# Performance work log

Hardware: AMD Instinct MI355X
Metric: run time of the kernel (lower is better)

## Reference

```python
import jax, jax.numpy as jnp
import numpy as np

ALPHA = 0.15
CLIP = 5.0
EPS = 1e-6
LN_EPS = 1e-5

B, S, D, F = 4, 4096, 2048, 128


def setup_inputs() -> dict:
    key = jax.random.key(0)
    ks = jax.random.split(key, 8)
    sd = lambda fan_in: 1.0 / np.sqrt(fan_in)
    return {
        "x": jax.random.normal(ks[0], (B, S, D), dtype=jnp.float32),
        "Q_w": jax.random.normal(ks[1], (D, F), dtype=jnp.float32) * sd(D),
        "Q_b": jnp.zeros((F,), jnp.float32),
        "K_w": jax.random.normal(ks[2], (D, F), dtype=jnp.float32) * sd(D),
        "K_b": jnp.zeros((F,), jnp.float32),
        "lo_proj_w": jax.random.normal(ks[3], (D, D), dtype=jnp.float32) * sd(D),
        "lo_proj_b": jnp.zeros((D,), jnp.float32),
        "lo_p_w": jax.random.normal(ks[4], (D, F), dtype=jnp.float32) * sd(D),
        "lo_p_b": jnp.zeros((F,), jnp.float32),
        "proj_w": jax.random.normal(ks[5], (F, D), dtype=jnp.float32) * sd(F),
        "proj_b": jnp.zeros((D,), jnp.float32),
        "O_w": jax.random.normal(ks[6], (D // 2, D), dtype=jnp.float32) * sd(D // 2),
        "O_b": jnp.zeros((D,), jnp.float32),
        "ln_gamma": jnp.ones((D,), jnp.float32),
        "ln_beta": jnp.zeros((D,), jnp.float32),
    }


def _ema_over_time(score):
    # score: [B, S, F]; ema[0]=score[0]; ema[t]=a*score[t]+(1-a)*ema[t-1]
    seq = jnp.swapaxes(score, 0, 1)  # [S, B, F]

    def step(prev, x_t):
        new = ALPHA * x_t + (1.0 - ALPHA) * prev
        return new, new

    init = seq[0]
    _, rest = jax.lax.scan(step, init, seq[1:])
    ema_seq = jnp.concatenate([init[None], rest], axis=0)
    return jnp.swapaxes(ema_seq, 0, 1)


def reference(x, Q_w, Q_b, K_w, K_b, lo_proj_w, lo_proj_b, lo_p_w, lo_p_b,
              proj_w, proj_b, O_w, O_b, ln_gamma, ln_beta):
    x_f32 = x.astype(jnp.float32)
    residual = x_f32

    q = x_f32 @ Q_w + Q_b                    # [B,S,128]
    k = x_f32 @ K_w + K_b                    # [B,S,128]
    # Lo: Dense(d_model) -> gelu -> Dense(128)
    v_h = jax.nn.gelu(x_f32 @ lo_proj_w + lo_proj_b)
    V = v_h @ lo_p_w + lo_p_b                # [B,S,128]

    score = jax.nn.sigmoid(q) * jax.nn.sigmoid(k)
    score_ema = _ema_over_time(score)
    mean_last = jnp.mean(score_ema, axis=-1, keepdims=True)
    denom = jnp.maximum(mean_last, EPS)
    score_clipped = jnp.clip(score_ema / denom, -CLIP, CLIP)

    x_comb = score_clipped * V               # [B,S,128]
    out = x_comb @ proj_w + proj_b           # [B,S,D]  (D even -> no pad)
    a, b = jnp.split(out, 2, axis=-1)
    gated = jax.nn.silu(a) * b               # [B,S,D/2]
    out = gated @ O_w + O_b                  # [B,S,D]

    h = out + residual
    mu = jnp.mean(h, axis=-1, keepdims=True)
    var = jnp.var(h, axis=-1, keepdims=True)
    out = (h - mu) * jax.lax.rsqrt(var + LN_EPS) * ln_gamma + ln_beta
    return out.astype(x.dtype)
```

## Files before the change

kernel.cpp:

```cpp
#include <hip/hip_runtime.h>
#include <cstdint>

#define ALPHA_C 0.15f
#define ONE_MINUS_ALPHA 0.85f
#define CLIP_C 5.0f
#define EPS_C 1e-6f
#define LN_EPS_C 1e-5f

#define Bb 4
#define Ss 4096
#define Dd 2048
#define Mtot (Bb * Ss)

typedef __attribute__((ext_vector_type(8))) short bf16x8;
typedef __attribute__((ext_vector_type(4))) float f32x4;

__device__ __forceinline__ short f2bf(float f) {
  union { float f; uint32_t u; } v; v.f = f;
  uint32_t r = v.u + 0x7fffu + ((v.u >> 16) & 1u);
  return (short)(r >> 16);
}
__device__ __forceinline__ float sigf(float x) { return 1.0f / (1.0f + __expf(-x)); }
__device__ __forceinline__ float geluf(float x) {
  const float c = 0.7978845608028654f;
  float x3 = x * x * x;
  return 0.5f * x * (1.0f + tanhf(c * (x + 0.044715f * x3)));
}

__device__ __forceinline__ void load_lds16(const short* g, short* l) {
  __builtin_amdgcn_global_load_lds((__attribute__((address_space(1))) void*)g,
                                   (__attribute__((address_space(3))) void*)l, 16, 0, 0);
}


#define RD_A(MH, KK)                                                                 \
  _Pragma("unroll") for (int mm = 0; mm < 4; ++mm)                                   \
      a[mm] = *(const bf16x8*)&Ab[(wr128 + ((MH) * 4 + mm) * 16 + l16) * 64 +        \
                                  ((((KK) * 4 + quad) ^ key) * 8)];
#define RD_B(KK)                                                                     \
  _Pragma("unroll") for (int nn = 0; nn < 4; ++nn)                                   \
      bq[nn] = *(const bf16x8*)&Bl[(wc64 + nn * 16 + l16) * 64 +                     \
                                   ((((KK) * 4 + quad) ^ key) * 8)];
#define MFMA_Q(MH)                                                                   \
  __builtin_amdgcn_s_setprio(1);                                                     \
  _Pragma("unroll") for (int mm = 0; mm < 4; ++mm)                                   \
  _Pragma("unroll") for (int nn = 0; nn < 4; ++nn)                                   \
      acc[(MH) * 4 + mm][nn] = __builtin_amdgcn_mfma_f32_16x16x32_bf16(              \
          a[mm], bq[nn], acc[(MH) * 4 + mm][nn], 0, 0, 0);                           \
  __builtin_amdgcn_s_setprio(0);
#define BARF()                                                                       \
  {                                                                                  \
    asm volatile("" ::: "memory");                                                   \
    __builtin_amdgcn_s_barrier();                                                    \
    asm volatile("" ::: "memory");                                                   \
  }
#define STAGE_HALF_A(TT, H)                                                          \
  {                                                                                  \
    short* ls = smem + ((TT) & 1) * 32768 + (H) * 8192;                              \
    const long co = (long)(TT) * 64;                                                 \
    load_lds16(baseA + ((H) * 128 + 0) * (long)lda + co, ls + w * 512);              \
    load_lds16(baseA + ((H) * 128 + 64) * (long)lda + co, ls + 4096 + w * 512);      \
  }
#define STAGE_HALF_B(TT, H)                                                          \
  {                                                                                  \
    short* ls = smem + ((TT) & 1) * 32768 + 16384 + (H) * 8192;                      \
    const long co = (long)(TT) * 64;                                                 \
    load_lds16(baseB + ((H) * 128 + 0) * (long)ldb + co, ls + w * 512);              \
    load_lds16(baseB + ((H) * 128 + 64) * (long)ldb + co, ls + 4096 + w * 512);      \
  }

#define TILE_BODY(CB, STG, TN)                                                       \
  {                                                                                  \
    const short* Ab = smem + (CB) * 32768;                                           \
    const short* Bl = Ab + 16384;                                                    \
                                                                  \
    if (STG) {                                                                       \
      STAGE_HALF_A(TN, 0);                                                           \
      asm volatile("s_waitcnt vmcnt(2)" ::: "memory");                               \
    } else {                                                                         \
      asm volatile("s_waitcnt vmcnt(0)" ::: "memory");                               \
    }                                                                                \
    __builtin_amdgcn_s_barrier();                                                    \
    asm volatile("" ::: "memory");                                                   \
    RD_A(0, 0);                                                                      \
    RD_B(0);                                                                         \
    asm volatile("s_waitcnt lgkmcnt(0)" ::: "memory");                               \
    MFMA_Q(0);                                                                       \
    BARF();                                                                          \
                                                                        \
    RD_A(1, 0);                                                                      \
    if (STG) STAGE_HALF_A(TN, 1);                                                    \
    __builtin_amdgcn_s_barrier();                                                    \
    asm volatile("s_waitcnt lgkmcnt(0)" ::: "memory");                               \
    MFMA_Q(1);                                                                       \
    BARF();                                                                          \
                                                                        \
    RD_A(0, 1);                                                                      \
    RD_B(1);                                                                         \
    if (STG) STAGE_HALF_B(TN, 0);                                                    \
    __builtin_amdgcn_s_barrier();                                                    \
    asm volatile("s_waitcnt lgkmcnt(0)" ::: "memory");                               \
    MFMA_Q(0);                                                                       \
    BARF();                                                                          \
                                                                        \
    RD_A(1, 1);                                                                      \
    if (STG) STAGE_HALF_B(TN, 1);                                                    \
    __builtin_amdgcn_s_barrier();                                                    \
    asm volatile("s_waitcnt lgkmcnt(0)" ::: "memory");                               \
    MFMA_Q(1);                                                                       \
    BARF();                                                                          \
  }

template <int MODE>
__global__ __launch_bounds__(512, 2) void gemm256(
    const short* __restrict__ A, const short* __restrict__ Bt, void* __restrict__ out0,
    void* __restrict__ out1, const float* __restrict__ bias, int K, int lda, int ldb,
    int ldc, int nbx) {
  __shared__ short smem[65536];

  const int tid = threadIdx.x;
  const int w = tid >> 6;
  const int lane = tid & 63;
  const int quad = lane >> 4;
  const int l16 = lane & 15;
  const int key = l16 & 7;
  const int wr = w >> 2;
  const int wc = w & 3;
  const int wr128 = wr * 128;
  const int wc64 = wc * 64;

  const int nwg = gridDim.x;
  const int swz = (blockIdx.x & 7) * (nwg >> 3) + (blockIdx.x >> 3);
  const int by = swz / nbx;
  const int bx = swz - by * nbx;
  const int m0 = by * 256;
  const int n0 = bx * 256;

  const int rowoff = lane >> 3;
  const int schunk = ((lane & 7) ^ (lane >> 3)) * 8;
  const short* baseA = A + (long)(m0 + w * 8 + rowoff) * lda + schunk;
  const short* baseB = Bt + (long)(n0 + w * 8 + rowoff) * ldb + schunk;

  const int NT = K >> 6;

  f32x4 acc[8][4] = {};
  bf16x8 a[4], bq[4];

  STAGE_HALF_A(0, 0);
  STAGE_HALF_A(0, 1);
  STAGE_HALF_B(0, 0);
  STAGE_HALF_B(0, 1);

  int t = 0;
  for (; t < NT - 2; t += 2) {
    TILE_BODY(0, 1, t + 1);
    TILE_BODY(1, 1, t + 2);
  }
  TILE_BODY(0, 1, t + 1);
  TILE_BODY(1, 0, 0);

#pragma unroll
  for (int m = 0; m < 8; ++m) {
#pragma unroll
    for (int r = 0; r < 4; ++r) {
      const int row = m0 + wr128 + m * 16 + quad * 4 + r;
#pragma unroll
      for (int n = 0; n < 4; ++n) {
        const int col = n0 + wc64 + n * 16 + l16;
        float v = acc[m][n][r] + bias[col];
        if (MODE == 0) {
          ((float*)out0)[(long)row * ldc + col] = v;
        } else {
          if (n0 == 0) {
            float sh = __shfl_xor(v, 1);
            if (!(lane & 1))
              ((float*)out0)[(long)row * 128 + (col >> 1)] = sigf(v) * sigf(sh);
          } else {
            ((short*)out1)[(long)row * 2048 + (col - 256)] = f2bf(geluf(v));
          }
        }
      }
    }
  }
}

#define BM 128
#define BN 128
#define BK 32

template <int MODE>
__global__ __launch_bounds__(256, 4) void gemm_tn(
    const short* __restrict__ A, const short* __restrict__ Bt, void* __restrict__ out0,
    void* __restrict__ out1, const float* __restrict__ bias, int K, int lda, int ldb,
    int ldc, int nbx, long pstride) {
  __shared__ __align__(16) short As[BM * BK];
  __shared__ __align__(16) short Bs[BN * BK];

  const int tid = threadIdx.x;
  const int wave = tid >> 6;
  const int lane = tid & 63;
  const int quad = lane >> 4;
  const int l16 = lane & 15;

  const int bid = blockIdx.x;
  const int panel = bid / (8 * nbx);
  const int rem = bid - panel * (8 * nbx);
  const int by = panel * 8 + (rem & 7);
  const int bx = rem >> 3;
  const int m0 = by * BM;
  const int n0 = bx * BN;
  const int wm = (wave & 1) * 64;
  const int wn = (wave >> 1) * 64;

  if (MODE == 5) {
    A += (long)blockIdx.y * K;
    Bt += (long)blockIdx.y * K;
  }

  const int srow = wave * 32 + (lane >> 2);
  const int skoff = ((lane & 3) ^ ((lane >> 3) & 3)) * 8;
  const short* agp = A + (long)(m0 + srow) * lda + skoff;
  const short* bgp = Bt + (long)(n0 + srow) * ldb + skoff;
  const short* agp2 = agp + (long)16 * lda;
  const short* bgp2 = bgp + (long)16 * ldb;
  short* al = As + (wave * 32) * BK;
  short* al2 = al + 16 * BK;
  short* bl = Bs + (wave * 32) * BK;
  short* bl2 = bl + 16 * BK;

  const int rsw = (l16 >> 1) & 3;

  f32x4 acc[4][4] = {};

  for (int k0 = 0; k0 < K; k0 += BK) {
    __syncthreads();
    load_lds16(agp + k0, al);
    load_lds16(agp2 + k0, al2);
    load_lds16(bgp + k0, bl);
    load_lds16(bgp2 + k0, bl2);
    __syncthreads();

    bf16x8 af[4], bfr[4];
#pragma unroll
    for (int i = 0; i < 4; ++i)
      af[i] = *(const bf16x8*)&As[(wm + i * 16 + l16) * BK + (quad ^ rsw) * 8];
#pragma unroll
    for (int j = 0; j < 4; ++j)
      bfr[j] = *(const bf16x8*)&Bs[(wn + j * 16 + l16) * BK + (quad ^ rsw) * 8];
#pragma unroll
    for (int i = 0; i < 4; ++i)
#pragma unroll
      for (int j = 0; j < 4; ++j)
        acc[i][j] = __builtin_amdgcn_mfma_f32_16x16x32_bf16(af[i], bfr[j], acc[i][j], 0, 0, 0);
  }

#pragma unroll
  for (int i = 0; i < 4; ++i) {
#pragma unroll
    for (int r = 0; r < 4; ++r) {
      const int row = m0 + wm + i * 16 + quad * 4 + r;
#pragma unroll
      for (int j = 0; j < 4; ++j) {
        const int col = n0 + wn + j * 16 + l16;
        float v = acc[i][j][r];
        if (MODE != 5) v += bias[col];
        if (MODE == 0) {
          ((float*)out0)[(long)row * ldc + col] = v;
        } else if (MODE == 5) {
          float* o = (float*)out0 + (long)blockIdx.y * pstride;
          o[(long)row * ldc + col] = v;
        } else if (MODE == 3) {
          if (n0 < 256) {
            float sh = __shfl_xor(v, 1);
            if (!(lane & 1))
              ((float*)out0)[(long)row * 128 + (col >> 1)] = sigf(v) * sigf(sh);
          } else {
            ((short*)out1)[(long)row * 2048 + (col - 256)] = f2bf(geluf(v));
          }
        } else if (MODE == 4) {
          float sh = __shfl_xor(v, 1);
          if (!(lane & 1))
            ((short*)out0)[(long)row * 1024 + (col >> 1)] = f2bf(v * sigf(v) * sh);
        }
      }
    }
  }
}

__global__ __launch_bounds__(256) void cast_x_kernel(const float* __restrict__ in,
                                                     short* __restrict__ out, long n4) {
  long i = (long)blockIdx.x * blockDim.x + threadIdx.x;
  const long stride = (long)gridDim.x * blockDim.x;
  for (; i < n4; i += stride) {
    float4 v = ((const float4*)in)[i];
    short4 o;
    o.x = f2bf(v.x); o.y = f2bf(v.y); o.z = f2bf(v.z); o.w = f2bf(v.w);
    ((short4*)out)[i] = o;
  }
}

template <int MAP>
__global__ __launch_bounds__(256) void tcast_kernel(const float* __restrict__ in,
                                                    short* __restrict__ out, int R, int C) {
  __shared__ float t[32][33];
  const int c0 = blockIdx.x * 32, r0 = blockIdx.y * 32;
  const int tx = threadIdx.x, ty = threadIdx.y;
#pragma unroll
  for (int i = 0; i < 32; i += 8)
    t[ty + i][tx] = in[(long)(r0 + ty + i) * C + (c0 + tx)];
  __syncthreads();
#pragma unroll
  for (int i = 0; i < 32; i += 8) {
    const int c = c0 + ty + i;
    const int orow = (MAP == 0) ? c
                   : (MAP == 1) ? 2 * c
                   : (MAP == 2) ? 2 * c + 1
                                : (c < 1024 ? 2 * c : 2 * (c - 1024) + 1);
    out[(long)orow * R + (r0 + tx)] = f2bf(t[tx][ty + i]);
  }
}

__global__ void pack_bias_kernel(const float* __restrict__ qb, const float* __restrict__ kb,
                                 const float* __restrict__ lob, float* __restrict__ o) {
  int i = blockIdx.x * 256 + threadIdx.x;
  if (i < 256) o[i] = (i & 1) ? kb[i >> 1] : qb[i >> 1];
  else if (i < 2304) o[i] = lob[i - 256];
}
__global__ void pack_pbias_kernel(const float* __restrict__ pjb, float* __restrict__ o) {
  int i = blockIdx.x * 256 + threadIdx.x;
  o[i] = (i & 1) ? pjb[1024 + (i >> 1)] : pjb[i >> 1];
}

#define SEG 64
#define WARM 96
__global__ __launch_bounds__(128) void ema_kernel(const float* __restrict__ score,
                                                  float* __restrict__ ema) {
  const int f = threadIdx.x;
  const int b = blockIdx.y;
  const int seg = blockIdx.x;
  const int t0 = seg * SEG;
  const int tstart = (t0 >= WARM) ? (t0 - WARM) : 0;
  const int tend = t0 + SEG;
  const float* __restrict__ base = score + (long)b * Ss * 128;
  float* __restrict__ eb = ema + (long)b * Ss * 128;

  float e = base[(long)tstart * 128 + f];
  if (seg == 0) eb[f] = e;

  int t = tstart + 1;
  const int CH = 8;
  const int nch = (tend - t) / CH;
  float cur[CH];
#pragma unroll
  for (int i = 0; i < CH; ++i) cur[i] = ALPHA_C * base[(long)(t + i) * 128 + f];
  for (int c = 0; c < nch; ++c) {
    float nxt[CH] = {};
    if (c + 1 < nch) {
#pragma unroll
      for (int i = 0; i < CH; ++i) nxt[i] = ALPHA_C * base[(long)(t + CH + i) * 128 + f];
    }
#pragma unroll
    for (int i = 0; i < CH; ++i) {
      e = fmaf(ONE_MINUS_ALPHA, e, cur[i]);
      const int tt = t + i;
      if (tt >= t0) eb[(long)tt * 128 + f] = e;
    }
#pragma unroll
    for (int i = 0; i < CH; ++i) cur[i] = nxt[i];
    t += CH;
  }
  for (; t < tend; ++t) {
    e = fmaf(ONE_MINUS_ALPHA, e, ALPHA_C * base[(long)t * 128 + f]);
    if (t >= t0) eb[(long)t * 128 + f] = e;
  }
}

__global__ __launch_bounds__(256) void comb_kernel(const float* __restrict__ ema,
                                                   const float* __restrict__ vpart,
                                                   const float* __restrict__ lob,
                                                   short* __restrict__ xcomb) {
  const int wv = threadIdx.x >> 6;
  const int lane = threadIdx.x & 63;
  const long row = (long)blockIdx.x * 4 + wv;
  const float* er = ema + row * 128;
  float e0 = er[lane], e1 = er[lane + 64];
  float s = e0 + e1;
#pragma unroll
  for (int m = 1; m < 64; m <<= 1) s += __shfl_xor(s, m, 64);
  const float denom = fmaxf(s * (1.0f / 128.0f), EPS_C);
  const float inv = 1.0f / denom;
  const float c0 = fminf(fmaxf(e0 * inv, -CLIP_C), CLIP_C);
  const float c1 = fminf(fmaxf(e1 * inv, -CLIP_C), CLIP_C);
  const long PS = (long)Mtot * 128;
  float va = lob[lane], vb = lob[lane + 64];
#pragma unroll
  for (int p = 0; p < 4; ++p) {
    va += vpart[p * PS + row * 128 + lane];
    vb += vpart[p * PS + row * 128 + lane + 64];
  }
  xcomb[row * 128 + lane] = f2bf(c0 * va);
  xcomb[row * 128 + 64 + lane] = f2bf(c1 * vb);
}

__global__ __launch_bounds__(256) void ln_kernel(float* __restrict__ io,
                                                 const float* __restrict__ x,
                                                 const float* __restrict__ gamma,
                                                 const float* __restrict__ beta) {
  const long row = blockIdx.x;
  const int tid = threadIdx.x;
  const int wv = tid >> 6, lane = tid & 63;
  float* rp = io + row * 2048;
  const float* xp = x + row * 2048;
  float4 v0 = ((const float4*)rp)[tid * 2];
  float4 v1 = ((const float4*)rp)[tid * 2 + 1];
  float4 x0 = ((const float4*)xp)[tid * 2];
  float4 x1 = ((const float4*)xp)[tid * 2 + 1];
  float h[8] = {v0.x + x0.x, v0.y + x0.y, v0.z + x0.z, v0.w + x0.w,
                v1.x + x1.x, v1.y + x1.y, v1.z + x1.z, v1.w + x1.w};
  float sum = 0.f, ss = 0.f;
#pragma unroll
  for (int i = 0; i < 8; ++i) { sum += h[i]; ss += h[i] * h[i]; }
#pragma unroll
  for (int m = 1; m < 64; m <<= 1) {
    sum += __shfl_xor(sum, m, 64);
    ss += __shfl_xor(ss, m, 64);
  }
  __shared__ float rs[4], rq[4];
  if (lane == 0) { rs[wv] = sum; rq[wv] = ss; }
  __syncthreads();
  sum = rs[0] + rs[1] + rs[2] + rs[3];
  ss = rq[0] + rq[1] + rq[2] + rq[3];
  const float mu = sum * (1.0f / 2048.0f);
  const float var = ss * (1.0f / 2048.0f) - mu * mu;
  const float rstd = rsqrtf(var + LN_EPS_C);
  const int c0 = tid * 8;
  float o[8];
#pragma unroll
  for (int i = 0; i < 8; ++i)
    o[i] = (h[i] - mu) * rstd * gamma[c0 + i] + beta[c0 + i];
  ((float4*)rp)[tid * 2]     = make_float4(o[0], o[1], o[2], o[3]);
  ((float4*)rp)[tid * 2 + 1] = make_float4(o[4], o[5], o[6], o[7]);
}

extern "C" void kernel_launch(void* const* d_in, const int* in_sizes, int n_in,
                              void* d_out, int out_size, void* d_ws, size_t ws_size,
                              hipStream_t stream) {
  const float* x         = (const float*)d_in[0];
  const float* Q_w       = (const float*)d_in[1];
  const float* Q_b       = (const float*)d_in[2];
  const float* K_w       = (const float*)d_in[3];
  const float* K_b       = (const float*)d_in[4];
  const float* lo_proj_w = (const float*)d_in[5];
  const float* lo_proj_b = (const float*)d_in[6];
  const float* lo_p_w    = (const float*)d_in[7];
  const float* lo_p_b    = (const float*)d_in[8];
  const float* proj_w    = (const float*)d_in[9];
  const float* proj_b    = (const float*)d_in[10];
  const float* O_w       = (const float*)d_in[11];
  const float* O_b       = (const float*)d_in[12];
  const float* ln_g      = (const float*)d_in[13];
  const float* ln_b      = (const float*)d_in[14];

  char* ws = (char*)d_ws;
  size_t off = 0;
  auto alloc = [&](size_t bytes) {
    char* p = ws + off;
    off += (bytes + 255) & ~(size_t)255;
    return p;
  };
  short* x16   = (short*)alloc((size_t)Mtot * Dd * 2);
  short* h16   = (short*)alloc((size_t)Mtot * Dd * 2);
  float* score = (float*)alloc((size_t)Mtot * 128 * 4);
  float* emab  = (float*)alloc((size_t)Mtot * 128 * 4);
  short* xcomb = (short*)alloc((size_t)Mtot * 128 * 2);
  short* gated = (short*)alloc((size_t)Mtot * 1024 * 2);
  short* wbig  = (short*)alloc((size_t)2304 * 2048 * 2);
  short* lpt   = (short*)alloc((size_t)128 * 2048 * 2);
  short* prjt  = (short*)alloc((size_t)2048 * 128 * 2);
  short* ot    = (short*)alloc((size_t)2048 * 1024 * 2);
  float* biasb = (float*)alloc(2304 * 4);
  float* pbias = (float*)alloc(2048 * 4);
  float* vpart = (float*)x16;
  float* outf  = (float*)d_out;

  cast_x_kernel<<<8192, 256, 0, stream>>>(x, x16, (long)Mtot * Dd / 4);
  tcast_kernel<1><<<dim3(4, 64), dim3(32, 8), 0, stream>>>(Q_w, wbig, 2048, 128);
  tcast_kernel<2><<<dim3(4, 64), dim3(32, 8), 0, stream>>>(K_w, wbig, 2048, 128);
  tcast_kernel<0><<<dim3(64, 64), dim3(32, 8), 0, stream>>>(lo_proj_w, wbig + 256 * 2048, 2048, 2048);
  tcast_kernel<0><<<dim3(4, 64), dim3(32, 8), 0, stream>>>(lo_p_w, lpt, 2048, 128);
  tcast_kernel<3><<<dim3(64, 4), dim3(32, 8), 0, stream>>>(proj_w, prjt, 128, 2048);
  tcast_kernel<0><<<dim3(64, 32), dim3(32, 8), 0, stream>>>(O_w, ot, 1024, 2048);
  pack_bias_kernel<<<9, 256, 0, stream>>>(Q_b, K_b, lo_proj_b, biasb);
  pack_pbias_kernel<<<8, 256, 0, stream>>>(proj_b, pbias);

  gemm256<3><<<576, 512, 0, stream>>>(x16, wbig, score, h16, biasb,
                                      2048, 2048, 2048, 0, 9);
  ema_kernel<<<dim3(Ss / SEG, 4), 128, 0, stream>>>(score, emab);
  gemm_tn<5><<<dim3(128, 4), 256, 0, stream>>>(h16, lpt, vpart, nullptr, nullptr,
                                               512, 2048, 2048, 128, 1, (long)Mtot * 128);
  comb_kernel<<<Mtot / 4, 256, 0, stream>>>(emab, vpart, lo_p_b, xcomb);
  gemm_tn<4><<<16 * 128, 256, 0, stream>>>(xcomb, prjt, gated, nullptr, pbias,
                                           128, 128, 128, 1024, 16, 0);
  gemm256<0><<<512, 512, 0, stream>>>(gated, ot, outf, nullptr, O_b,
                                      1024, 1024, 1024, 2048, 8);
  ln_kernel<<<Mtot, 256, 0, stream>>>(outf, x, ln_g, ln_b);
}
```

Before: 721.1 us.

## Restructure GEMM LDS layout into K-halves with inline-asm reads and finer staging

Changes the LDS tile layout so each 64-wide K tile is stored as two 32-wide K-halves, with each thread staging contiguous 16-byte chunks. The XOR swizzle is dropped and ds_read_b128 is issued through inline asm on precomputed byte addresses. B fragments are now held per K-half, so each is read once instead of being reloaded. Global loads are staged per K-half and gated with vmcnt(4), with a sched_barrier after each lgkmcnt wait. The goal is less address arithmetic, fewer LDS reads and better overlap of loads with MFMA, at the cost of possible LDS bank conflicts now that the swizzle is gone and more registers for B.

```diff
diff --git a/kernel.cpp b/kernel.cpp
--- a/kernel.cpp
+++ b/kernel.cpp
@@ -32,83 +32,96 @@
                                    (__attribute__((address_space(3))) void*)l, 16, 0, 0);
 }
 
-
-#define RD_A(MH, KK)                                                                 \
-  _Pragma("unroll") for (int mm = 0; mm < 4; ++mm)                                   \
-      a[mm] = *(const bf16x8*)&Ab[(wr128 + ((MH) * 4 + mm) * 16 + l16) * 64 +        \
-                                  ((((KK) * 4 + quad) ^ key) * 8)];
-#define RD_B(KK)                                                                     \
-  _Pragma("unroll") for (int nn = 0; nn < 4; ++nn)                                   \
-      bq[nn] = *(const bf16x8*)&Bl[(wc64 + nn * 16 + l16) * 64 +                     \
-                                   ((((KK) * 4 + quad) ^ key) * 8)];
-#define MFMA_Q(MH)                                                                   \
-  __builtin_amdgcn_s_setprio(1);                                                     \
-  _Pragma("unroll") for (int mm = 0; mm < 4; ++mm)                                   \
-  _Pragma("unroll") for (int nn = 0; nn < 4; ++nn)                                   \
-      acc[(MH) * 4 + mm][nn] = __builtin_amdgcn_mfma_f32_16x16x32_bf16(              \
-          a[mm], bq[nn], acc[(MH) * 4 + mm][nn], 0, 0, 0);                           \
-  __builtin_amdgcn_s_setprio(0);
-#define BARF()                                                                       \
+__device__ __forceinline__ bf16x8 lds_rd128(uint32_t byteaddr) {
+  bf16x8 r;
+  asm volatile("ds_read_b128 %0, %1" : "=v"(r) : "v"(byteaddr));
+  return r;
+}
+
+
+#define BAR()                                                                        \
   {                                                                                  \
     asm volatile("" ::: "memory");                                                   \
     __builtin_amdgcn_s_barrier();                                                    \
     asm volatile("" ::: "memory");                                                   \
   }
-#define STAGE_HALF_A(TT, H)                                                          \
+#define GATE4() asm volatile("s_waitcnt vmcnt(4)" ::: "memory")
+#define GATE0() asm volatile("s_waitcnt vmcnt(0)" ::: "memory")
+#define LGKM0()                                                                      \
   {                                                                                  \
-    short* ls = smem + ((TT) & 1) * 32768 + (H) * 8192;                              \
-    const long co = (long)(TT) * 64;                                                 \
-    load_lds16(baseA + ((H) * 128 + 0) * (long)lda + co, ls + w * 512);              \
-    load_lds16(baseA + ((H) * 128 + 64) * (long)lda + co, ls + 4096 + w * 512);      \
-  }
-#define STAGE_HALF_B(TT, H)                                                          \
+    asm volatile("s_waitcnt lgkmcnt(0)" ::: "memory");                               \
+    __builtin_amdgcn_sched_barrier(0);                                               \
+  }
+
+#define RDA4(BUF, KK, MH)                                                            \
+  _Pragma("unroll") for (int mm = 0; mm < 4; ++mm)                                   \
+      a[mm] = lds_rd128(aA + (BUF)*65536u + (KK)*16384u + ((MH)*4 + mm) * 1024u);
+#define RDB4(BUF, KK)                                                                \
+  _Pragma("unroll") for (int nn = 0; nn < 4; ++nn)                                   \
+      bq[KK][nn] = lds_rd128(aB2 + (BUF)*65536u + (KK)*16384u + nn * 1024u);
+#define MFMAQ(MH, KK)                                                                \
+  __builtin_amdgcn_s_setprio(1);                                                     \
+  _Pragma("unroll") for (int mm = 0; mm < 4; ++mm)                                   \
+  _Pragma("unroll") for (int nn = 0; nn < 4; ++nn)                                   \
+      acc[(MH)*4 + mm][nn] = __builtin_amdgcn_mfma_f32_16x16x32_bf16(                \
+          a[mm], bq[KK][nn], acc[(MH)*4 + mm][nn], 0, 0, 0);                         \
+  __builtin_amdgcn_s_setprio(0);
+
+#define STG_A(TT, KK)                                                                \
   {                                                                                  \
-    short* ls = smem + ((TT) & 1) * 32768 + 16384 + (H) * 8192;                      \
-    const long co = (long)(TT) * 64;                                                 \
-    load_lds16(baseB + ((H) * 128 + 0) * (long)ldb + co, ls + w * 512);              \
-    load_lds16(baseB + ((H) * 128 + 64) * (long)ldb + co, ls + 4096 + w * 512);      \
+    load_lds16(aStage + (long)(KK)*32 + (long)(TT)*64,                               \
+               smem + (((TT)&1) * 32768 + (KK)*8192 + tid * 8));                     \
+    load_lds16(aStage + (long)128 * lda + (KK)*32 + (long)(TT)*64,                   \
+               smem + (((TT)&1) * 32768 + (KK)*8192 + 4096 + tid * 8));              \
+  }
+#define STG_B(TT, KK)                                                                \
+  {                                                                                  \
+    load_lds16(bStage + (long)(KK)*32 + (long)(TT)*64,                               \
+               smem + (((TT)&1) * 32768 + 16384 + (KK)*8192 + tid * 8));             \
+    load_lds16(bStage + (long)128 * ldb + (KK)*32 + (long)(TT)*64,                   \
+               smem + (((TT)&1) * 32768 + 16384 + (KK)*8192 + 4096 + tid * 8));      \
   }
 
 #define TILE_BODY(CB, STG, TN)                                                       \
   {                                                                                  \
-    const short* Ab = smem + (CB) * 32768;                                           \
-    const short* Bl = Ab + 16384;                                                    \
-                                                                  \
+                                                      \
+    RDA4(CB, 0, 0);                                                                  \
+    RDB4(CB, 0);                                                                     \
+    if (STG) STG_A(TN, 0);                                                           \
+    BAR();                                                                           \
+    LGKM0();                                                                         \
+    MFMAQ(0, 0);                                                                     \
+    BAR();                                                                           \
+                                                              \
+    RDA4(CB, 0, 1);                                                                  \
     if (STG) {                                                                       \
-      STAGE_HALF_A(TN, 0);                                                           \
-      asm volatile("s_waitcnt vmcnt(2)" ::: "memory");                               \
+      STG_B(TN, 0);                                                                  \
+      GATE4();                                                                       \
     } else {                                                                         \
-      asm volatile("s_waitcnt vmcnt(0)" ::: "memory");                               \
+      GATE0();                                                                       \
     }                                                                                \
-    __builtin_amdgcn_s_barrier();                                                    \
-    asm volatile("" ::: "memory");                                                   \
-    RD_A(0, 0);                                                                      \
-    RD_B(0);                                                                         \
-    asm volatile("s_waitcnt lgkmcnt(0)" ::: "memory");                               \
-    MFMA_Q(0);                                                                       \
-    BARF();                                                                          \
-                                                                        \
-    RD_A(1, 0);                                                                      \
-    if (STG) STAGE_HALF_A(TN, 1);                                                    \
-    __builtin_amdgcn_s_barrier();                                                    \
-    asm volatile("s_waitcnt lgkmcnt(0)" ::: "memory");                               \
-    MFMA_Q(1);                                                                       \
-    BARF();                                                                          \
-                                                                        \
-    RD_A(0, 1);                                                                      \
-    RD_B(1);                                                                         \
-    if (STG) STAGE_HALF_B(TN, 0);                                                    \
-    __builtin_amdgcn_s_barrier();                                                    \
-    asm volatile("s_waitcnt lgkmcnt(0)" ::: "memory");                               \
-    MFMA_Q(0);                                                                       \
-    BARF();                                                                          \
-                                                                        \
-    RD_A(1, 1);                                                                      \
-    if (STG) STAGE_HALF_B(TN, 1);                                                    \
-    __builtin_amdgcn_s_barrier();                                                    \
-    asm volatile("s_waitcnt lgkmcnt(0)" ::: "memory");                               \
-    MFMA_Q(1);                                                                       \
-    BARF();                                                                          \
+    BAR();                                                                           \
+    LGKM0();                                                                         \
+    MFMAQ(1, 0);                                                                     \
+    BAR();                                                                           \
+                                                              \
+    RDA4(CB, 1, 0);                                                                  \
+    RDB4(CB, 1);                                                                     \
+    if (STG) STG_A(TN, 1);                                                           \
+    BAR();                                                                           \
+    LGKM0();                                                                         \
+    MFMAQ(0, 1);                                                                     \
+    BAR();                                                                           \
+                                                              \
+    RDA4(CB, 1, 1);                                                                  \
+    if (STG) {                                                                       \
+      STG_B(TN, 1);                                                                  \
+      GATE4();                                                                       \
+    }                                                                                \
+    BAR();                                                                           \
+    LGKM0();                                                                         \
+    MFMAQ(1, 1);                                                                     \
+    BAR();                                                                           \
   }
 
 template <int MODE>
@@ -116,14 +129,13 @@
     const short* __restrict__ A, const short* __restrict__ Bt, void* __restrict__ out0,
     void* __restrict__ out1, const float* __restrict__ bias, int K, int lda, int ldb,
     int ldc, int nbx) {
-  __shared__ short smem[65536];
+  __shared__ __align__(16) short smem[65536];
 
   const int tid = threadIdx.x;
   const int w = tid >> 6;
   const int lane = tid & 63;
   const int quad = lane >> 4;
   const int l16 = lane & 15;
-  const int key = l16 & 7;
   const int wr = w >> 2;
   const int wc = w & 3;
   const int wr128 = wr * 128;
@@ -136,27 +148,31 @@
   const int m0 = by * 256;
   const int n0 = bx * 256;
 
-  const int rowoff = lane >> 3;
-  const int schunk = ((lane & 7) ^ (lane >> 3)) * 8;
-  const short* baseA = A + (long)(m0 + w * 8 + rowoff) * lda + schunk;
-  const short* baseB = Bt + (long)(n0 + w * 8 + rowoff) * ldb + schunk;
+  const short* aStage = A + (long)(m0 + (tid >> 2)) * lda + (tid & 3) * 8;
+  const short* bStage = Bt + (long)(n0 + (tid >> 2)) * ldb + (tid & 3) * 8;
+
+  const uint32_t sb = (uint32_t)(uintptr_t)smem;
+  const uint32_t aA = sb + (uint32_t)((wr128 + l16) * 64 + quad * 16);
+  const uint32_t aB2 = sb + 32768u + (uint32_t)((wc64 + l16) * 64 + quad * 16);
 
   const int NT = K >> 6;
 
   f32x4 acc[8][4] = {};
-  bf16x8 a[4], bq[4];
-
-  STAGE_HALF_A(0, 0);
-  STAGE_HALF_A(0, 1);
-  STAGE_HALF_B(0, 0);
-  STAGE_HALF_B(0, 1);
+  bf16x8 a[4], bq[2][4];
+
+  STG_A(0, 0);
+  STG_B(0, 0);
+  STG_A(0, 1);
+  STG_B(0, 1);
+  GATE4();
+  BAR();
 
   int t = 0;
   for (; t < NT - 2; t += 2) {
     TILE_BODY(0, 1, t + 1);
     TILE_BODY(1, 1, t + 2);
   }
-  TILE_BODY(0, 1, t + 1);
+  TILE_BODY(0, 1, NT - 1);
   TILE_BODY(1, 0, 0);
 
 #pragma unroll
```

Result: slower. 968.1 us (+34.2%).
